# Kernel tuning notes

Measured on AMD Instinct MI355X. Metric: run time of the kernel, lower is better.

## Reference

```python
import jax, jax.numpy as jnp
import numpy as np

N_NODES = 50000
N_EDGES = 800000
IN_CH = 128
HID = 256
NUM_LAYERS = 3


def setup_inputs() -> dict:
    key = jax.random.key(0)
    ks = jax.random.split(key, 16)
    x = jax.random.normal(ks[0], (N_NODES, IN_CH), dtype=jnp.float32)
    edge_index = jax.random.randint(ks[1], (2, N_EDGES), 0, N_NODES, dtype=jnp.int64)
    inp = {"x": x, "edge_index": edge_index}
    dims = [(IN_CH, HID), (HID, HID), (HID, HID)]
    for i, (din, dout) in enumerate(dims):
        s = 1.0 / np.sqrt(din)
        # lin_l (applied to aggregated neighbors, has bias), lin_r (root, no bias)
        inp[f"Wl{i}"] = jax.random.uniform(ks[2 + 3 * i], (din, dout), jnp.float32, -s, s)
        inp[f"b{i}"] = jax.random.uniform(ks[3 + 3 * i], (dout,), jnp.float32, -s, s)
        inp[f"Wr{i}"] = jax.random.uniform(ks[4 + 3 * i], (din, dout), jnp.float32, -s, s)
    return inp


def _sage_layer(x, src, dst, Wl, b, Wr):
    # mean aggregation of source-node features at destination nodes
    msg = x[src]  # [E, din]
    summed = jax.ops.segment_sum(msg, dst, num_segments=N_NODES)
    cnt = jax.ops.segment_sum(jnp.ones((src.shape[0], 1), x.dtype), dst, num_segments=N_NODES)
    agg = summed / jnp.maximum(cnt, 1.0)
    return agg @ Wl + b + x @ Wr


def reference(x, edge_index, Wl0, b0, Wr0, Wl1, b1, Wr1, Wl2, b2, Wr2):
    src, dst = edge_index[0], edge_index[1]
    params = [(Wl0, b0, Wr0), (Wl1, b1, Wr1), (Wl2, b2, Wr2)]
    h = x
    for i, (Wl, b, Wr) in enumerate(params):
        h = _sage_layer(h, src, dst, Wl, b, Wr)
        if i < NUM_LAYERS - 1:
            h = jax.nn.relu(h)  # dropout p=0.0 -> identity
    return h
```

## Files before the change

### kernel.cpp

```cpp
#include <hip/hip_runtime.h>
#include <hip/hip_bf16.h>

#define N_NODES 50000
#define N_EDGES 800000
#define MBLKS ((N_NODES + 255) / 256)
#define XCD_RANGE 6250
#define SLOT_CAP 64
#define EDGE_GROUP_BLOCKS 200

typedef __attribute__((ext_vector_type(4))) float f32x4;
typedef __attribute__((ext_vector_type(16))) float f32x16;
typedef __attribute__((ext_vector_type(8))) short s16x8;

__device__ int   g_cursor[N_NODES];
__device__ __attribute__((aligned(256))) int g_adjf[(size_t)N_NODES * SLOT_CAP];
__device__ __attribute__((aligned(256))) unsigned short g_aggbf[(size_t)N_NODES * 256];
__device__ __attribute__((aligned(256))) unsigned short g_bf0[(size_t)N_NODES * 256];
__device__ __attribute__((aligned(256))) unsigned short g_bf1[(size_t)N_NODES * 256];
__device__ __attribute__((aligned(256))) unsigned short g_Whi[6][256 * 256];
__device__ __attribute__((aligned(256))) unsigned short g_Wlo[6][256 * 256];

__device__ __forceinline__ unsigned short f2bf(float f) {
    unsigned int u = __float_as_uint(f);
    unsigned int r = (u + 0x7fffu + ((u >> 16) & 1u)) >> 16;
    return (unsigned short)r;
}
__device__ __forceinline__ float bf2f(unsigned short h) {
    return __uint_as_float(((unsigned int)h) << 16);
}

__global__ void zero_kernel() {
    int i = blockIdx.x * blockDim.x + threadIdx.x;
    if (i < N_NODES) g_cursor[i] = 0;
}

__device__ __forceinline__ void prep_w_seg(const float* __restrict__ W, int K,
                                           int widx, int lbx, int tid) {
    int e = lbx * 256 + tid;
    if (e >= K * 256) return;
    int k = e >> 8, n = e & 255;
    float w = W[e];
    unsigned short hi = f2bf(w);
    unsigned short lo = f2bf(w - bf2f(hi));
    g_Whi[widx][n * K + k] = hi;
    g_Wlo[widx][n * K + k] = lo;
}

__global__ void build_prep_kernel(const int* __restrict__ ei, const float* __restrict__ x,
                                  const float* __restrict__ Wl0, const float* __restrict__ Wr0,
                                  const float* __restrict__ Wl1, const float* __restrict__ Wr1,
                                  const float* __restrict__ Wl2, const float* __restrict__ Wr2) {
    int bx = blockIdx.x;
    int tid = threadIdx.x;
    if (bx < 8 * EDGE_GROUP_BLOCKS) {
        const int grp = bx & 7;
        const int gbx = bx >> 3;
        const int lo = grp * XCD_RANGE, hi = lo + XCD_RANGE;
        const int NQ = N_EDGES / 4;
        for (int q = gbx * 256 + tid; q < NQ; q += EDGE_GROUP_BLOCKS * 256) {
            int4 s4 = *(const int4*)(ei + q * 4);
            int4 d4 = *(const int4*)(ei + N_EDGES + q * 4);
            if (d4.x >= lo && d4.x < hi) {
                int p = atomicAdd(&g_cursor[d4.x], 1);
                if (p < SLOT_CAP) g_adjf[(long)d4.x * SLOT_CAP + p] = ((unsigned)s4.x < N_NODES) ? s4.x : 0;
            }
            if (d4.y >= lo && d4.y < hi) {
                int p = atomicAdd(&g_cursor[d4.y], 1);
                if (p < SLOT_CAP) g_adjf[(long)d4.y * SLOT_CAP + p] = ((unsigned)s4.y < N_NODES) ? s4.y : 0;
            }
            if (d4.z >= lo && d4.z < hi) {
                int p = atomicAdd(&g_cursor[d4.z], 1);
                if (p < SLOT_CAP) g_adjf[(long)d4.z * SLOT_CAP + p] = ((unsigned)s4.z < N_NODES) ? s4.z : 0;
            }
            if (d4.w >= lo && d4.w < hi) {
                int p = atomicAdd(&g_cursor[d4.w], 1);
                if (p < SLOT_CAP) g_adjf[(long)d4.w * SLOT_CAP + p] = ((unsigned)s4.w < N_NODES) ? s4.w : 0;
            }
        }
        return;
    }
    bx -= 8 * EDGE_GROUP_BLOCKS;
    if (bx < 128)   { prep_w_seg(Wl0, 128, 0, bx, tid);        return; }
    if (bx < 256)   { prep_w_seg(Wr0, 128, 1, bx - 128, tid);  return; }
    if (bx < 512)   { prep_w_seg(Wl1, 256, 2, bx - 256, tid);  return; }
    if (bx < 768)   { prep_w_seg(Wr1, 256, 3, bx - 512, tid);  return; }
    if (bx < 1024)  { prep_w_seg(Wl2, 256, 4, bx - 768, tid);  return; }
    if (bx < 1280)  { prep_w_seg(Wr2, 256, 5, bx - 1024, tid); return; }
    long i = (long)(bx - 1280) * 256 + tid;
    if (i >= (long)N_NODES * 128 / 8) return;
    const float* xp = x + i * 8;
    f32x4 v0 = *(const f32x4*)(xp);
    f32x4 v1 = *(const f32x4*)(xp + 4);
    s16x8 o;
    o[0] = (short)f2bf(v0.x); o[1] = (short)f2bf(v0.y);
    o[2] = (short)f2bf(v0.z); o[3] = (short)f2bf(v0.w);
    o[4] = (short)f2bf(v1.x); o[5] = (short)f2bf(v1.y);
    o[6] = (short)f2bf(v1.z); o[7] = (short)f2bf(v1.w);
    *(s16x8*)(g_bf0 + i * 8) = o;
}

template <int DIN>
__global__ __launch_bounds__(256) void agg_wave_kernel(int sel) {
    const unsigned short* __restrict__ hb = sel == 0 ? g_bf0 : g_bf1;
    constexpr int LPR = DIN / 8;
    constexpr int RPW = 64 / LPR;
    const int node = blockIdx.x * 4 + (threadIdx.x >> 6);
    if (node >= N_NODES) return;
    const int lane = threadIdx.x & 63;
    const int rg = lane / LPR;
    const int cl = lane % LPR;
    const int cnt = g_cursor[node];
    const int e = (cnt < SLOT_CAP) ? cnt : SLOT_CAP;
    const int* __restrict__ adj = g_adjf + (long)node * SLOT_CAP;

    float acc[8];
#pragma unroll
    for (int j = 0; j < 8; ++j) acc[j] = 0.f;

    int i = 0;
    for (; i + 8 * RPW <= e; i += 8 * RPW) {
        int a[8];
#pragma unroll
        for (int u = 0; u < 8; ++u) a[u] = adj[i + u * RPW + rg];
        s16x8 v[8];
#pragma unroll
        for (int u = 0; u < 8; ++u) v[u] = *(const s16x8*)(hb + (long)a[u] * DIN + cl * 8);
#pragma unroll
        for (int u = 0; u < 8; ++u)
#pragma unroll
            for (int j = 0; j < 8; ++j) acc[j] += bf2f((unsigned short)v[u][j]);
    }
    for (; i + 4 * RPW <= e; i += 4 * RPW) {
        int a[4];
#pragma unroll
        for (int u = 0; u < 4; ++u) a[u] = adj[i + u * RPW + rg];
        s16x8 v[4];
#pragma unroll
        for (int u = 0; u < 4; ++u) v[u] = *(const s16x8*)(hb + (long)a[u] * DIN + cl * 8);
#pragma unroll
        for (int u = 0; u < 4; ++u)
#pragma unroll
            for (int j = 0; j < 8; ++j) acc[j] += bf2f((unsigned short)v[u][j]);
    }
    for (; i < e; i += RPW) {
        int eidx = i + rg;
        if (eidx < e) {
            int a = adj[eidx];
            s16x8 v = *(const s16x8*)(hb + (long)a * DIN + cl * 8);
#pragma unroll
            for (int j = 0; j < 8; ++j) acc[j] += bf2f((unsigned short)v[j]);
        }
    }

#pragma unroll
    for (int j = 0; j < 8; ++j) {
        if (RPW == 4) acc[j] += __shfl_xor(acc[j], 16, 64);
        acc[j] += __shfl_xor(acc[j], 32, 64);
    }

    if (rg == 0) {
        float inv = 1.f / fmaxf((float)cnt, 1.f);
        s16x8 ov;
#pragma unroll
        for (int j = 0; j < 8; ++j) ov[j] = (short)f2bf(acc[j] * inv);
        *(s16x8*)(g_aggbf + (long)node * DIN + cl * 8) = ov;
    }
}

template <int K, bool RELU, bool FP32OUT>
__global__ __launch_bounds__(256, 3) void gemm2_mfma(
    int a2_sel, int widx, const float* __restrict__ bias,
    float* __restrict__ outp, int bfsel) {
    __shared__ __attribute__((aligned(16))) char lds[49152];
    char* const As = lds;
    char* const Wh = lds + 32768;
    char* const Wl = lds + 40960;

    const int tid = threadIdx.x;
    const int w = tid >> 6;
    const int l = tid & 63;
    const int l31 = l & 31;
    const int lh = l >> 5;
    const int bx = blockIdx.x;
    const int xcd = bx & 7;
    const int idx = bx >> 3;
    const int mblk = (idx >> 2) * 8 + xcd;
    const int nblk = idx & 3;
    if (mblk >= MBLKS) return;
    const long row0 = (long)mblk * 256;
    const int ncol0 = nblk * 64;

    f32x16 acc[2][2];
#pragma unroll
    for (int i = 0; i < 2; ++i)
#pragma unroll
        for (int j = 0; j < 2; ++j) acc[i][j] = (f32x16)0.f;

    const int sar = tid >> 3;
    const int sac = tid & 7;
    const int swn = tid >> 2;
    const int swc = (tid & 3) * 2;

    const unsigned short* A2p = a2_sel == 0 ? (const unsigned short*)g_bf0
                                            : (const unsigned short*)g_bf1;
    constexpr int NPP = K / 64;
    constexpr int NT = NPP * 2;

    s16x8 aR[8], whR[2], wlR[2];
    auto issue = [&](int t) {
        int pass = (t >= NPP) ? 1 : 0;
        int kc = (t - pass * NPP) * 64;
        const unsigned short* A = pass ? A2p : (const unsigned short*)g_aggbf;
        const unsigned short* WH = g_Whi[widx + pass] + (long)ncol0 * K;
        const unsigned short* WL = g_Wlo[widx + pass] + (long)ncol0 * K;
#pragma unroll
        for (int j = 0; j < 8; ++j) {
            int r = j * 32 + sar;
            long grow = row0 + r; if (grow > N_NODES - 1) grow = N_NODES - 1;
            aR[j] = *(const s16x8*)(A + grow * K + kc + sac * 8);
        }
#pragma unroll
        for (int q = 0; q < 2; ++q) {
            int c = swc + q;
            whR[q] = *(const s16x8*)(WH + (long)swn * K + kc + c * 8);
            wlR[q] = *(const s16x8*)(WL + (long)swn * K + kc + c * 8);
        }
    };

    issue(0);
    for (int t = 0; t < NT; ++t) {
#pragma unroll
        for (int j = 0; j < 8; ++j) {
            int r = j * 32 + sar;
            *(s16x8*)(As + r * 128 + ((sac * 16) ^ ((r & 7) << 4))) = aR[j];
        }
#pragma unroll
        for (int q = 0; q < 2; ++q) {
            int c = swc + q;
            int o = swn * 128 + ((c * 16) ^ ((swn & 7) << 4));
            *(s16x8*)(Wh + o) = whR[q];
            *(s16x8*)(Wl + o) = wlR[q];
        }
        __syncthreads();
        if (t + 1 < NT) issue(t + 1);
#pragma unroll
        for (int ks = 0; ks < 4; ++ks) {
            const int kb = ks * 32 + lh * 16;
            s16x8 af[2], bh[2], bl[2];
#pragma unroll
            for (int mi = 0; mi < 2; ++mi) {
                int r = w * 64 + mi * 32 + l31;
                af[mi] = *(const s16x8*)(As + r * 128 + (kb ^ ((r & 7) << 4)));
            }
#pragma unroll
            for (int ni = 0; ni < 2; ++ni) {
                int n = ni * 32 + l31;
                int o = n * 128 + (kb ^ ((n & 7) << 4));
                bh[ni] = *(const s16x8*)(Wh + o);
                bl[ni] = *(const s16x8*)(Wl + o);
            }
#pragma unroll
            for (int mi = 0; mi < 2; ++mi)
#pragma unroll
                for (int ni = 0; ni < 2; ++ni)
                    acc[mi][ni] = __builtin_amdgcn_mfma_f32_32x32x16_bf16(af[mi], bh[ni], acc[mi][ni], 0, 0, 0);
#pragma unroll
            for (int mi = 0; mi < 2; ++mi)
#pragma unroll
                for (int ni = 0; ni < 2; ++ni)
                    acc[mi][ni] = __builtin_amdgcn_mfma_f32_32x32x16_bf16(af[mi], bl[ni], acc[mi][ni], 0, 0, 0);
        }
        __syncthreads();
    }

    unsigned short* bfout = bfsel == 0 ? g_bf0 : g_bf1;
#pragma unroll
    for (int ni = 0; ni < 2; ++ni) {
        int col = ncol0 + ni * 32 + l31;
        float bv = bias[col];
#pragma unroll
        for (int mi = 0; mi < 2; ++mi) {
#pragma unroll
            for (int reg = 0; reg < 16; ++reg) {
                int lr = (reg & 3) + 8 * (reg >> 2) + 4 * lh;
                long grow = row0 + w * 64 + mi * 32 + lr;
                if (grow < N_NODES) {
                    float v = acc[mi][ni][reg] + bv;
                    if (RELU) v = fmaxf(v, 0.f);
                    if (FP32OUT) outp[grow * 256 + col] = v;
                    else bfout[grow * 256 + col] = f2bf(v);
                }
            }
        }
    }
}

extern "C" void kernel_launch(void* const* d_in, const int* in_sizes, int n_in,
                              void* d_out, int out_size, void* d_ws, size_t ws_size,
                              hipStream_t stream) {
    const float* x = (const float*)d_in[0];
    const int* ei = (const int*)d_in[1];
    const float* Wl0 = (const float*)d_in[2];
    const float* b0  = (const float*)d_in[3];
    const float* Wr0 = (const float*)d_in[4];
    const float* Wl1 = (const float*)d_in[5];
    const float* b1  = (const float*)d_in[6];
    const float* Wr1 = (const float*)d_in[7];
    const float* Wl2 = (const float*)d_in[8];
    const float* b2  = (const float*)d_in[9];
    const float* Wr2 = (const float*)d_in[10];
    float* out = (float*)d_out;

    int nblocks = (N_NODES + 255) / 256;

    zero_kernel<<<nblocks, 256, 0, stream>>>();
    build_prep_kernel<<<8 * EDGE_GROUP_BLOCKS + 1280 + 3125, 256, 0, stream>>>(
        ei, x, Wl0, Wr0, Wl1, Wr1, Wl2, Wr2);

    int gblocks = 800;
    int ablocks = (N_NODES + 3) / 4;

    agg_wave_kernel<128><<<ablocks, 256, 0, stream>>>(0);
    gemm2_mfma<128, true, false><<<gblocks, 256, 0, stream>>>(0, 0, b0, nullptr, 1);

    agg_wave_kernel<256><<<ablocks, 256, 0, stream>>>(1);
    gemm2_mfma<256, true, false><<<gblocks, 256, 0, stream>>>(1, 2, b1, nullptr, 0);

    agg_wave_kernel<256><<<ablocks, 256, 0, stream>>>(0);
    gemm2_mfma<256, false, true><<<gblocks, 256, 0, stream>>>(0, 4, b2, out, 1);
}
```

Before: 329.9 us.

## Overlap root GEMM with neighbor aggregation in one launch, split GEMM passes

Moves the root-term GEMM (x @ Wr + b) into the aggregation kernel as extra blocks, so the bandwidth-bound gather and the compute-bound root GEMM run concurrently in one grid. The root result is written to a new fp32 buffer, and the second GEMM (agg @ Wl) adds it in its epilogue. This hides aggregation latency behind MFMA work. In exchange it adds an fp32 round trip through global memory of N_NODES*256 floats per layer, and the fused kernel carries 48KB of LDS with a launch bound of 3 blocks, which may limit aggregation occupancy.

```diff
diff --git a/kernel.cpp b/kernel.cpp
--- a/kernel.cpp
+++ b/kernel.cpp
@@ -7,6 +7,8 @@
 #define XCD_RANGE 6250
 #define SLOT_CAP 64
 #define EDGE_GROUP_BLOCKS 200
+#define ABLOCKS ((N_NODES + 3) / 4)
+#define GBLOCKS 800
 
 typedef __attribute__((ext_vector_type(4))) float f32x4;
 typedef __attribute__((ext_vector_type(16))) float f32x16;
@@ -17,6 +19,7 @@
 __device__ __attribute__((aligned(256))) unsigned short g_aggbf[(size_t)N_NODES * 256];
 __device__ __attribute__((aligned(256))) unsigned short g_bf0[(size_t)N_NODES * 256];
 __device__ __attribute__((aligned(256))) unsigned short g_bf1[(size_t)N_NODES * 256];
+__device__ __attribute__((aligned(256))) float g_root[(size_t)N_NODES * 256];
 __device__ __attribute__((aligned(256))) unsigned short g_Whi[6][256 * 256];
 __device__ __attribute__((aligned(256))) unsigned short g_Wlo[6][256 * 256];
 
@@ -99,78 +102,197 @@
     *(s16x8*)(g_bf0 + i * 8) = o;
 }
 
-template <int DIN>
-__global__ __launch_bounds__(256) void agg_wave_kernel(int sel) {
+template <int K>
+__global__ __launch_bounds__(256, 3) void fused_agg_root(
+    int sel, int widx, const float* __restrict__ bias) {
+    __shared__ __attribute__((aligned(16))) char lds[49152];
+
     const unsigned short* __restrict__ hb = sel == 0 ? g_bf0 : g_bf1;
-    constexpr int LPR = DIN / 8;
-    constexpr int RPW = 64 / LPR;
-    const int node = blockIdx.x * 4 + (threadIdx.x >> 6);
-    if (node >= N_NODES) return;
-    const int lane = threadIdx.x & 63;
-    const int rg = lane / LPR;
-    const int cl = lane % LPR;
-    const int cnt = g_cursor[node];
-    const int e = (cnt < SLOT_CAP) ? cnt : SLOT_CAP;
-    const int* __restrict__ adj = g_adjf + (long)node * SLOT_CAP;
-
-    float acc[8];
-#pragma unroll
-    for (int j = 0; j < 8; ++j) acc[j] = 0.f;
-
-    int i = 0;
-    for (; i + 8 * RPW <= e; i += 8 * RPW) {
-        int a[8];
-#pragma unroll
-        for (int u = 0; u < 8; ++u) a[u] = adj[i + u * RPW + rg];
-        s16x8 v[8];
-#pragma unroll
-        for (int u = 0; u < 8; ++u) v[u] = *(const s16x8*)(hb + (long)a[u] * DIN + cl * 8);
-#pragma unroll
-        for (int u = 0; u < 8; ++u)
-#pragma unroll
-            for (int j = 0; j < 8; ++j) acc[j] += bf2f((unsigned short)v[u][j]);
-    }
-    for (; i + 4 * RPW <= e; i += 4 * RPW) {
-        int a[4];
-#pragma unroll
-        for (int u = 0; u < 4; ++u) a[u] = adj[i + u * RPW + rg];
-        s16x8 v[4];
-#pragma unroll
-        for (int u = 0; u < 4; ++u) v[u] = *(const s16x8*)(hb + (long)a[u] * DIN + cl * 8);
-#pragma unroll
-        for (int u = 0; u < 4; ++u)
-#pragma unroll
-            for (int j = 0; j < 8; ++j) acc[j] += bf2f((unsigned short)v[u][j]);
-    }
-    for (; i < e; i += RPW) {
-        int eidx = i + rg;
-        if (eidx < e) {
-            int a = adj[eidx];
-            s16x8 v = *(const s16x8*)(hb + (long)a * DIN + cl * 8);
-#pragma unroll
-            for (int j = 0; j < 8; ++j) acc[j] += bf2f((unsigned short)v[j]);
-        }
-    }
-
-#pragma unroll
-    for (int j = 0; j < 8; ++j) {
-        if (RPW == 4) acc[j] += __shfl_xor(acc[j], 16, 64);
-        acc[j] += __shfl_xor(acc[j], 32, 64);
-    }
-
-    if (rg == 0) {
-        float inv = 1.f / fmaxf((float)cnt, 1.f);
-        s16x8 ov;
-#pragma unroll
-        for (int j = 0; j < 8; ++j) ov[j] = (short)f2bf(acc[j] * inv);
-        *(s16x8*)(g_aggbf + (long)node * DIN + cl * 8) = ov;
+    const int bxg = blockIdx.x;
+
+    if (bxg < ABLOCKS) {
+        constexpr int LPR = K / 8;
+        constexpr int RPW = 64 / LPR;
+        const int node = bxg * 4 + (threadIdx.x >> 6);
+        if (node >= N_NODES) return;
+        const int lane = threadIdx.x & 63;
+        const int rg = lane / LPR;
+        const int cl = lane % LPR;
+        const int cnt = g_cursor[node];
+        const int e = (cnt < SLOT_CAP) ? cnt : SLOT_CAP;
+        const int* __restrict__ adj = g_adjf + (long)node * SLOT_CAP;
+
+        float acc[8];
+#pragma unroll
+        for (int j = 0; j < 8; ++j) acc[j] = 0.f;
+
+        int i = 0;
+        for (; i + 8 * RPW <= e; i += 8 * RPW) {
+            int a[8];
+#pragma unroll
+            for (int u = 0; u < 8; ++u) a[u] = adj[i + u * RPW + rg];
+            s16x8 v[8];
+#pragma unroll
+            for (int u = 0; u < 8; ++u) v[u] = *(const s16x8*)(hb + (long)a[u] * K + cl * 8);
+#pragma unroll
+            for (int u = 0; u < 8; ++u)
+#pragma unroll
+                for (int j = 0; j < 8; ++j) acc[j] += bf2f((unsigned short)v[u][j]);
+        }
+        for (; i + 4 * RPW <= e; i += 4 * RPW) {
+            int a[4];
+#pragma unroll
+            for (int u = 0; u < 4; ++u) a[u] = adj[i + u * RPW + rg];
+            s16x8 v[4];
+#pragma unroll
+            for (int u = 0; u < 4; ++u) v[u] = *(const s16x8*)(hb + (long)a[u] * K + cl * 8);
+#pragma unroll
+            for (int u = 0; u < 4; ++u)
+#pragma unroll
+                for (int j = 0; j < 8; ++j) acc[j] += bf2f((unsigned short)v[u][j]);
+        }
+        for (; i < e; i += RPW) {
+            int eidx = i + rg;
+            if (eidx < e) {
+                int a = adj[eidx];
+                s16x8 v = *(const s16x8*)(hb + (long)a * K + cl * 8);
+#pragma unroll
+                for (int j = 0; j < 8; ++j) acc[j] += bf2f((unsigned short)v[j]);
+            }
+        }
+
+#pragma unroll
+        for (int j = 0; j < 8; ++j) {
+            if (RPW == 4) acc[j] += __shfl_xor(acc[j], 16, 64);
+            acc[j] += __shfl_xor(acc[j], 32, 64);
+        }
+
+        if (rg == 0) {
+            float inv = 1.f / fmaxf((float)cnt, 1.f);
+            s16x8 ov;
+#pragma unroll
+            for (int j = 0; j < 8; ++j) ov[j] = (short)f2bf(acc[j] * inv);
+            *(s16x8*)(g_aggbf + (long)node * K + cl * 8) = ov;
+        }
+        return;
+    }
+
+    char* const As = lds;
+    char* const Wh = lds + 32768;
+    char* const Wl = lds + 40960;
+
+    const int tid = threadIdx.x;
+    const int w = tid >> 6;
+    const int l = tid & 63;
+    const int l31 = l & 31;
+    const int lh = l >> 5;
+    const int gi = bxg - ABLOCKS;
+    const int xcd = gi & 7;
+    const int idx = gi >> 3;
+    const int mblk = (idx >> 2) * 8 + xcd;
+    const int nblk = idx & 3;
+    if (mblk >= MBLKS) return;
+    const long row0 = (long)mblk * 256;
+    const int ncol0 = nblk * 64;
+
+    f32x16 acc[2][2];
+#pragma unroll
+    for (int i = 0; i < 2; ++i)
+#pragma unroll
+        for (int j = 0; j < 2; ++j) acc[i][j] = (f32x16)0.f;
+
+    const int sar = tid >> 3;
+    const int sac = tid & 7;
+    const int swn = tid >> 2;
+    const int swc = (tid & 3) * 2;
+
+    const unsigned short* WH = g_Whi[widx] + (long)ncol0 * K;
+    const unsigned short* WL = g_Wlo[widx] + (long)ncol0 * K;
+    constexpr int NT = K / 64;
+
+    s16x8 aR[8], whR[2], wlR[2];
+    auto issue = [&](int t) {
+        int kc = t * 64;
+#pragma unroll
+        for (int j = 0; j < 8; ++j) {
+            int r = j * 32 + sar;
+            long grow = row0 + r; if (grow > N_NODES - 1) grow = N_NODES - 1;
+            aR[j] = *(const s16x8*)(hb + grow * K + kc + sac * 8);
+        }
+#pragma unroll
+        for (int q = 0; q < 2; ++q) {
+            int c = swc + q;
+            whR[q] = *(const s16x8*)(WH + (long)swn * K + kc + c * 8);
+            wlR[q] = *(const s16x8*)(WL + (long)swn * K + kc + c * 8);
+        }
+    };
+
+    issue(0);
+    for (int t = 0; t < NT; ++t) {
+#pragma unroll
+        for (int j = 0; j < 8; ++j) {
+            int r = j * 32 + sar;
+            *(s16x8*)(As + r * 128 + ((sac * 16) ^ ((r & 7) << 4))) = aR[j];
+        }
+#pragma unroll
+        for (int q = 0; q < 2; ++q) {
+            int c = swc + q;
+            int o = swn * 128 + ((c * 16) ^ ((swn & 7) << 4));
+            *(s16x8*)(Wh + o) = whR[q];
+            *(s16x8*)(Wl + o) = wlR[q];
+        }
+        __syncthreads();
+        if (t + 1 < NT) issue(t + 1);
+#pragma unroll
+        for (int ks = 0; ks < 4; ++ks) {
+            const int kb = ks * 32 + lh * 16;
+            s16x8 af[2], bh[2], bl[2];
+#pragma unroll
+            for (int mi = 0; mi < 2; ++mi) {
+                int r = w * 64 + mi * 32 + l31;
+                af[mi] = *(const s16x8*)(As + r * 128 + (kb ^ ((r & 7) << 4)));
+            }
+#pragma unroll
+            for (int ni = 0; ni < 2; ++ni) {
+                int n = ni * 32 + l31;
+                int o = n * 128 + (kb ^ ((n & 7) << 4));
+                bh[ni] = *(const s16x8*)(Wh + o);
+                bl[ni] = *(const s16x8*)(Wl + o);
+            }
+#pragma unroll
+            for (int mi = 0; mi < 2; ++mi)
+#pragma unroll
+                for (int ni = 0; ni < 2; ++ni)
+                    acc[mi][ni] = __builtin_amdgcn_mfma_f32_32x32x16_bf16(af[mi], bh[ni], acc[mi][ni], 0, 0, 0);
+#pragma unroll
+            for (int mi = 0; mi < 2; ++mi)
+#pragma unroll
+                for (int ni = 0; ni < 2; ++ni)
+                    acc[mi][ni] = __builtin_amdgcn_mfma_f32_32x32x16_bf16(af[mi], bl[ni], acc[mi][ni], 0, 0, 0);
+        }
+        __syncthreads();
+    }
+
+#pragma unroll
+    for (int ni = 0; ni < 2; ++ni) {
+        int col = ncol0 + ni * 32 + l31;
+        float bv = bias[col];
+#pragma unroll
+        for (int mi = 0; mi < 2; ++mi) {
+#pragma unroll
+            for (int reg = 0; reg < 16; ++reg) {
+                int lr = (reg & 3) + 8 * (reg >> 2) + 4 * lh;
+                long grow = row0 + w * 64 + mi * 32 + lr;
+                if (grow < N_NODES)
+                    g_root[grow * 256 + col] = acc[mi][ni][reg] + bv;
+            }
+        }
     }
 }
 
 template <int K, bool RELU, bool FP32OUT>
-__global__ __launch_bounds__(256, 3) void gemm2_mfma(
-    int a2_sel, int widx, const float* __restrict__ bias,
-    float* __restrict__ outp, int bfsel) {
+__global__ __launch_bounds__(256, 3) void gemm_agg(
+    int widx, float* __restrict__ outp, int bfsel) {
     __shared__ __attribute__((aligned(16))) char lds[49152];
     char* const As = lds;
     char* const Wh = lds + 32768;
@@ -201,18 +323,14 @@
     const int swn = tid >> 2;
     const int swc = (tid & 3) * 2;
 
-    const unsigned short* A2p = a2_sel == 0 ? (const unsigned short*)g_bf0
-                                            : (const unsigned short*)g_bf1;
-    constexpr int NPP = K / 64;
-    constexpr int NT = NPP * 2;
+    const unsigned short* A = g_aggbf;
+    const unsigned short* WH = g_Whi[widx] + (long)ncol0 * K;
+    const unsigned short* WL = g_Wlo[widx] + (long)ncol0 * K;
+    constexpr int NT = K / 64;
 
     s16x8 aR[8], whR[2], wlR[2];
     auto issue = [&](int t) {
-        int pass = (t >= NPP) ? 1 : 0;
-        int kc = (t - pass * NPP) * 64;
-        const unsigned short* A = pass ? A2p : (const unsigned short*)g_aggbf;
-        const unsigned short* WH = g_Whi[widx + pass] + (long)ncol0 * K;
-        const unsigned short* WL = g_Wlo[widx + pass] + (long)ncol0 * K;
+        int kc = t * 64;
 #pragma unroll
         for (int j = 0; j < 8; ++j) {
             int r = j * 32 + sar;
@@ -277,7 +395,6 @@
 #pragma unroll
     for (int ni = 0; ni < 2; ++ni) {
         int col = ncol0 + ni * 32 + l31;
-        float bv = bias[col];
 #pragma unroll
         for (int mi = 0; mi < 2; ++mi) {
 #pragma unroll
@@ -285,7 +402,7 @@
                 int lr = (reg & 3) + 8 * (reg >> 2) + 4 * lh;
                 long grow = row0 + w * 64 + mi * 32 + lr;
                 if (grow < N_NODES) {
-                    float v = acc[mi][ni][reg] + bv;
+                    float v = acc[mi][ni][reg] + g_root[grow * 256 + col];
                     if (RELU) v = fmaxf(v, 0.f);
                     if (FP32OUT) outp[grow * 256 + col] = v;
                     else bfout[grow * 256 + col] = f2bf(v);
@@ -317,15 +434,12 @@
     build_prep_kernel<<<8 * EDGE_GROUP_BLOCKS + 1280 + 3125, 256, 0, stream>>>(
         ei, x, Wl0, Wr0, Wl1, Wr1, Wl2, Wr2);
 
-    int gblocks = 800;
-    int ablocks = (N_NODES + 3) / 4;
-
-    agg_wave_kernel<128><<<ablocks, 256, 0, stream>>>(0);
-    gemm2_mfma<128, true, false><<<gblocks, 256, 0, stream>>>(0, 0, b0, nullptr, 1);
-
-    agg_wave_kernel<256><<<ablocks, 256, 0, stream>>>(1);
-    gemm2_mfma<256, true, false><<<gblocks, 256, 0, stream>>>(1, 2, b1, nullptr, 0);
-
-    agg_wave_kernel<256><<<ablocks, 256, 0, stream>>>(0);
-    gemm2_mfma<256, false, true><<<gblocks, 256, 0, stream>>>(0, 4, b2, out, 1);
-}
+    fused_agg_root<128><<<ABLOCKS + GBLOCKS, 256, 0, stream>>>(0, 1, b0);
+    gemm_agg<128, true, false><<<GBLOCKS, 256, 0, stream>>>(0, nullptr, 1);
+
+    fused_agg_root<256><<<ABLOCKS + GBLOCKS, 256, 0, stream>>>(1, 3, b1);
+    gemm_agg<256, true, false><<<GBLOCKS, 256, 0, stream>>>(2, nullptr, 0);
+
+    fused_agg_root<256><<<ABLOCKS + GBLOCKS, 256, 0, stream>>>(0, 5, b2);
+    gemm_agg<256, false, true><<<GBLOCKS, 256, 0, stream>>>(4, out, 1);
+}
```

Result: slower. 485.0 us (+47.0%).

## Replace LDS-staged GEMM with direct global-to-register MFMA operand loads

Applied to the files above, without the earlier changes.

The GEMM kernel no longer stages A and weight tiles through shared memory with barriers and a register prefetch. Each lane now loads its MFMA operand fragments straight from global memory and relies on cache for reuse across waves. This removes the LDS writes, the LDS reads and the __syncthreads barriers. In exchange it loses explicit prefetch overlap, may cause redundant global or L2 traffic for the weights, and reads row-strided operands with 16-byte accesses.

```diff
diff --git a/kernel.cpp b/kernel.cpp
--- a/kernel.cpp
+++ b/kernel.cpp
@@ -7,6 +7,7 @@
 #define XCD_RANGE 6250
 #define SLOT_CAP 64
 #define EDGE_GROUP_BLOCKS 200
+#define GBLOCKS 800
 
 typedef __attribute__((ext_vector_type(4))) float f32x4;
 typedef __attribute__((ext_vector_type(16))) float f32x16;
@@ -168,14 +169,9 @@
 }
 
 template <int K, bool RELU, bool FP32OUT>
-__global__ __launch_bounds__(256, 3) void gemm2_mfma(
+__global__ __launch_bounds__(256, 3) void gemm2_nolds(
     int a2_sel, int widx, const float* __restrict__ bias,
     float* __restrict__ outp, int bfsel) {
-    __shared__ __attribute__((aligned(16))) char lds[49152];
-    char* const As = lds;
-    char* const Wh = lds + 32768;
-    char* const Wl = lds + 40960;
-
     const int tid = threadIdx.x;
     const int w = tid >> 6;
     const int l = tid & 63;
@@ -196,81 +192,41 @@
 #pragma unroll
         for (int j = 0; j < 2; ++j) acc[i][j] = (f32x16)0.f;
 
-    const int sar = tid >> 3;
-    const int sac = tid & 7;
-    const int swn = tid >> 2;
-    const int swc = (tid & 3) * 2;
+    long ar0 = row0 + w * 64 + l31;      if (ar0 > N_NODES - 1) ar0 = N_NODES - 1;
+    long ar1 = ar0 + 32;                 if (ar1 > N_NODES - 1) ar1 = N_NODES - 1;
+    const int kofs = lh * 8;
 
     const unsigned short* A2p = a2_sel == 0 ? (const unsigned short*)g_bf0
                                             : (const unsigned short*)g_bf1;
-    constexpr int NPP = K / 64;
-    constexpr int NT = NPP * 2;
-
-    s16x8 aR[8], whR[2], wlR[2];
-    auto issue = [&](int t) {
-        int pass = (t >= NPP) ? 1 : 0;
-        int kc = (t - pass * NPP) * 64;
+
+#pragma unroll
+    for (int pass = 0; pass < 2; ++pass) {
         const unsigned short* A = pass ? A2p : (const unsigned short*)g_aggbf;
         const unsigned short* WH = g_Whi[widx + pass] + (long)ncol0 * K;
         const unsigned short* WL = g_Wlo[widx + pass] + (long)ncol0 * K;
-#pragma unroll
-        for (int j = 0; j < 8; ++j) {
-            int r = j * 32 + sar;
-            long grow = row0 + r; if (grow > N_NODES - 1) grow = N_NODES - 1;
-            aR[j] = *(const s16x8*)(A + grow * K + kc + sac * 8);
-        }
-#pragma unroll
-        for (int q = 0; q < 2; ++q) {
-            int c = swc + q;
-            whR[q] = *(const s16x8*)(WH + (long)swn * K + kc + c * 8);
-            wlR[q] = *(const s16x8*)(WL + (long)swn * K + kc + c * 8);
-        }
-    };
-
-    issue(0);
-    for (int t = 0; t < NT; ++t) {
-#pragma unroll
-        for (int j = 0; j < 8; ++j) {
-            int r = j * 32 + sar;
-            *(s16x8*)(As + r * 128 + ((sac * 16) ^ ((r & 7) << 4))) = aR[j];
-        }
-#pragma unroll
-        for (int q = 0; q < 2; ++q) {
-            int c = swc + q;
-            int o = swn * 128 + ((c * 16) ^ ((swn & 7) << 4));
-            *(s16x8*)(Wh + o) = whR[q];
-            *(s16x8*)(Wl + o) = wlR[q];
-        }
-        __syncthreads();
-        if (t + 1 < NT) issue(t + 1);
-#pragma unroll
-        for (int ks = 0; ks < 4; ++ks) {
-            const int kb = ks * 32 + lh * 16;
-            s16x8 af[2], bh[2], bl[2];
-#pragma unroll
-            for (int mi = 0; mi < 2; ++mi) {
-                int r = w * 64 + mi * 32 + l31;
-                af[mi] = *(const s16x8*)(As + r * 128 + (kb ^ ((r & 7) << 4)));
-            }
-#pragma unroll
-            for (int ni = 0; ni < 2; ++ni) {
-                int n = ni * 32 + l31;
-                int o = n * 128 + (kb ^ ((n & 7) << 4));
-                bh[ni] = *(const s16x8*)(Wh + o);
-                bl[ni] = *(const s16x8*)(Wl + o);
-            }
-#pragma unroll
-            for (int mi = 0; mi < 2; ++mi)
-#pragma unroll
-                for (int ni = 0; ni < 2; ++ni)
-                    acc[mi][ni] = __builtin_amdgcn_mfma_f32_32x32x16_bf16(af[mi], bh[ni], acc[mi][ni], 0, 0, 0);
-#pragma unroll
-            for (int mi = 0; mi < 2; ++mi)
-#pragma unroll
-                for (int ni = 0; ni < 2; ++ni)
-                    acc[mi][ni] = __builtin_amdgcn_mfma_f32_32x32x16_bf16(af[mi], bl[ni], acc[mi][ni], 0, 0, 0);
-        }
-        __syncthreads();
+        const unsigned short* a0p = A + ar0 * K + kofs;
+        const unsigned short* a1p = A + ar1 * K + kofs;
+        const unsigned short* w0h = WH + (long)l31 * K + kofs;
+        const unsigned short* w1h = WH + (long)(32 + l31) * K + kofs;
+        const unsigned short* w0l = WL + (long)l31 * K + kofs;
+        const unsigned short* w1l = WL + (long)(32 + l31) * K + kofs;
+#pragma unroll 4
+        for (int kk = 0; kk < K; kk += 16) {
+            s16x8 af0 = *(const s16x8*)(a0p + kk);
+            s16x8 af1 = *(const s16x8*)(a1p + kk);
+            s16x8 b0h = *(const s16x8*)(w0h + kk);
+            s16x8 b1h = *(const s16x8*)(w1h + kk);
+            s16x8 b0l = *(const s16x8*)(w0l + kk);
+            s16x8 b1l = *(const s16x8*)(w1l + kk);
+            acc[0][0] = __builtin_amdgcn_mfma_f32_32x32x16_bf16(af0, b0h, acc[0][0], 0, 0, 0);
+            acc[0][1] = __builtin_amdgcn_mfma_f32_32x32x16_bf16(af0, b1h, acc[0][1], 0, 0, 0);
+            acc[1][0] = __builtin_amdgcn_mfma_f32_32x32x16_bf16(af1, b0h, acc[1][0], 0, 0, 0);
+            acc[1][1] = __builtin_amdgcn_mfma_f32_32x32x16_bf16(af1, b1h, acc[1][1], 0, 0, 0);
+            acc[0][0] = __builtin_amdgcn_mfma_f32_32x32x16_bf16(af0, b0l, acc[0][0], 0, 0, 0);
+            acc[0][1] = __builtin_amdgcn_mfma_f32_32x32x16_bf16(af0, b1l, acc[0][1], 0, 0, 0);
+            acc[1][0] = __builtin_amdgcn_mfma_f32_32x32x16_bf16(af1, b0l, acc[1][0], 0, 0, 0);
+            acc[1][1] = __builtin_amdgcn_mfma_f32_32x32x16_bf16(af1, b1l, acc[1][1], 0, 0, 0);
+        }
     }
 
     unsigned short* bfout = bfsel == 0 ? g_bf0 : g_bf1;
@@ -312,20 +268,18 @@
     float* out = (float*)d_out;
 
     int nblocks = (N_NODES + 255) / 256;
+    int ablocks = (N_NODES + 3) / 4;
 
     zero_kernel<<<nblocks, 256, 0, stream>>>();
     build_prep_kernel<<<8 * EDGE_GROUP_BLOCKS + 1280 + 3125, 256, 0, stream>>>(
         ei, x, Wl0, Wr0, Wl1, Wr1, Wl2, Wr2);
 
-    int gblocks = 800;
-    int ablocks = (N_NODES + 3) / 4;
-
     agg_wave_kernel<128><<<ablocks, 256, 0, stream>>>(0);
-    gemm2_mfma<128, true, false><<<gblocks, 256, 0, stream>>>(0, 0, b0, nullptr, 1);
+    gemm2_nolds<128, true, false><<<GBLOCKS, 256, 0, stream>>>(0, 0, b0, nullptr, 1);
 
     agg_wave_kernel<256><<<ablocks, 256, 0, stream>>>(1);
-    gemm2_mfma<256, true, false><<<gblocks, 256, 0, stream>>>(1, 2, b1, nullptr, 0);
+    gemm2_nolds<256, true, false><<<GBLOCKS, 256, 0, stream>>>(1, 2, b1, nullptr, 0);
 
     agg_wave_kernel<256><<<ablocks, 256, 0, stream>>>(0);
-    gemm2_mfma<256, false, true><<<gblocks, 256, 0, stream>>>(0, 4, b2, out, 1);
-}
+    gemm2_nolds<256, false, true><<<GBLOCKS, 256, 0, stream>>>(0, 4, b2, out, 1);
+}
```

Measured after the change: 451.0 us. +36.7%, slower.
